# Performance work log

Hardware: AMD Instinct MI355X
Metric: run time of the kernel (lower is better)

Reference implementation:

```python
import jax, jax.numpy as jnp
import numpy as np

D_MODEL = 1024
NUM_HEADS = 16


def _linear(x, W, b):
    # torch nn.Linear: y = x @ W.T + b
    return jnp.einsum('bsd,od->bso', x, W) + b


def _split_heads(x, H):
    B, S, D = x.shape
    return x.reshape(B, S, H, D // H).transpose(0, 2, 1, 3)  # [B,H,S,dk]


def setup_inputs() -> dict:
    key0 = jax.random.key(0)
    ks = jax.random.split(key0, 11)
    B, S, D = 4, 2048, D_MODEL
    w_scale = 1.0 / np.sqrt(D)
    inp = {
        'query': jax.random.normal(ks[0], (B, S, D), jnp.float32),
        'key': jax.random.normal(ks[1], (B, S, D), jnp.float32),
        'value': jax.random.normal(ks[2], (B, S, D), jnp.float32),
        'Wq': jax.random.normal(ks[3], (D, D), jnp.float32) * w_scale,
        'bq': jax.random.normal(ks[4], (D,), jnp.float32) * 0.01,
        'Wk': jax.random.normal(ks[5], (D, D), jnp.float32) * w_scale,
        'bk': jax.random.normal(ks[6], (D,), jnp.float32) * 0.01,
        'Wv': jax.random.normal(ks[7], (D, D), jnp.float32) * w_scale,
        'bv': jax.random.normal(ks[8], (D,), jnp.float32) * 0.01,
        'Wo': jax.random.normal(ks[9], (D, D), jnp.float32) * w_scale,
        'bo': jax.random.normal(ks[10], (D,), jnp.float32) * 0.01,
        'common_prefix_len': 1792,
    }
    return inp


def reference(query, key, value, Wq, bq, Wk, bk, Wv, bv, Wo, bo, common_prefix_len):
    B, S, D = query.shape
    H = NUM_HEADS
    dk = D // H
    P = common_prefix_len
    scale = 1.0 / np.sqrt(dk)

    Q = _split_heads(_linear(query, Wq, bq), H)  # [B,H,S,dk]
    K = _split_heads(_linear(key, Wk, bk), H)
    V = _split_heads(_linear(value, Wv, bv), H)

    # --- prefix: causal self-attention over first P tokens ---
    Qp, Kp, Vp = Q[:, :, :P], K[:, :, :P], V[:, :, :P]
    sp = jnp.einsum('bhld,bhsd->bhls', Qp, Kp) * scale  # [B,H,P,P]
    causal = jnp.tril(jnp.ones((P, P), dtype=bool))
    sp = jnp.where(causal, sp, -jnp.inf)
    prefix_ctx = jnp.einsum('bhls,bhsd->bhld', jax.nn.softmax(sp, axis=-1), Vp)

    # --- candidates: attend to full prefix + own diagonal entry ---
    Qc = Q[:, :, P:]  # [B,H,N,dk]
    N = S - P
    sc = jnp.einsum('bhld,bhsd->bhls', Qc, K) * scale  # [B,H,N,S]
    mask = jnp.concatenate(
        [jnp.ones((N, P), dtype=bool), jnp.eye(N, dtype=bool)], axis=-1)  # [N,S]
    sc = jnp.where(mask, sc, -jnp.inf)
    cand_ctx = jnp.einsum('bhls,bhsd->bhld', jax.nn.softmax(sc, axis=-1), V)

    ctx = jnp.concatenate([prefix_ctx, cand_ctx], axis=2)  # [B,H,S,dk]
    ctx = ctx.transpose(0, 2, 1, 3).reshape(B, S, D)
    return _linear(ctx, Wo, bo)
```

## Files before the change

### kernel.cpp

```cpp
#include <hip/hip_runtime.h>
#include <hip/hip_bf16.h>
#include <stdint.h>
#include <stddef.h>

#define D_M   1024
#define N_H   16
#define D_K   64
#define S_LEN 2048
#define N_B   4
#define P_LEN 1792
#define M_ROWS (N_B*S_LEN)

#define QSCALE 0.1803368801111601f

typedef unsigned short u16;
typedef __bf16  bf16x8 __attribute__((ext_vector_type(8)));
typedef __bf16  bf16x4 __attribute__((ext_vector_type(4)));
typedef __bf16  bf16x2 __attribute__((ext_vector_type(2)));
typedef float   f32x4  __attribute__((ext_vector_type(4)));
typedef float   f32x16 __attribute__((ext_vector_type(16)));
typedef unsigned u32x4 __attribute__((ext_vector_type(4)));

#define MFMA32(a,b,c)   __builtin_amdgcn_mfma_f32_16x16x32_bf16((a),(b),(c),0,0,0)
#define MFMA3216(a,b,c) __builtin_amdgcn_mfma_f32_32x32x16_bf16((a),(b),(c),0,0,0)

__device__ __forceinline__ float ex2(float x){
#if defined(__HIP_DEVICE_COMPILE__) && __has_builtin(__builtin_amdgcn_exp2f)
  return __builtin_amdgcn_exp2f(x);
#else
  return exp2f(x);
#endif
}

#define GLDS16(gp, lp) __builtin_amdgcn_global_load_lds( \
    (__attribute__((address_space(1))) void*)(gp), \
    (__attribute__((address_space(3))) void*)(lp), 16, 0, 0)

__device__ __forceinline__ u16 f2bf(float f){
  unsigned u = __builtin_bit_cast(unsigned, f);
  u += 0x7FFFu + ((u>>16)&1u);
  return (u16)(u>>16);
}

__device__ __forceinline__ unsigned pkbf(float a, float b){
  bf16x2 t; t[0] = (__bf16)a; t[1] = (__bf16)b;
  return __builtin_bit_cast(unsigned, t);
}

__device__ __forceinline__ void plswap(unsigned &x, unsigned &y){
  asm("v_permlane32_swap_b32 %0, %1" : "+v"(x), "+v"(y));
}

__global__ void cvt4_bf16(const float* __restrict__ w0, const float* __restrict__ w1,
                          const float* __restrict__ w2, const float* __restrict__ w3,
                          u16* __restrict__ wqkv, u16* __restrict__ wo){
  typedef u16 u16x8 __attribute__((ext_vector_type(8)));
  const float* in = (blockIdx.y==0)? w0 : (blockIdx.y==1)? w1 : (blockIdx.y==2)? w2 : w3;
  u16* o8 = (blockIdx.y==3) ? wo : (wqkv + ((size_t)blockIdx.y << 20));
  const int i = blockIdx.x*blockDim.x + threadIdx.x;
  const float4* p = (const float4*)(in + (size_t)i*8);
  float4 a = p[0], b = p[1];
  u16x8 o;
  o[0]=f2bf(a.x); o[1]=f2bf(a.y); o[2]=f2bf(a.z); o[3]=f2bf(a.w);
  o[4]=f2bf(b.x); o[5]=f2bf(b.y); o[6]=f2bf(b.z); o[7]=f2bf(b.w);
  *(u16x8*)(o8 + (size_t)i*8) = o;
}

__global__ __launch_bounds__(256,3)
void gemm_qkv(const float* __restrict__ Aq, const float* __restrict__ Ak,
              const float* __restrict__ Av, const u16* __restrict__ W,
              const float* __restrict__ bqp, const float* __restrict__ bkp,
              const float* __restrict__ bvp,
              u16* __restrict__ Qo, u16* __restrict__ Ko, u16* __restrict__ Vo)
{
  constexpr int Kd = 1024, NT = Kd/32;
  __shared__ __align__(16) float AsF[128*32];
  __shared__ __align__(16) u16   Bs[128*32];
  const int tid  = threadIdx.x;
  const int wid  = tid >> 6, lane = tid & 63;
  const int z    = blockIdx.z;
  const int rowBase = blockIdx.x * 128, colBase = blockIdx.y * 128;

  const float* A32  = (z==0)? Aq : (z==1)? Ak : Av;
  const u16*   Bm   = W + ((size_t)z << 20);
  const float* bias = (z==0)? bqp : (z==1)? bkp : bvp;
  const float  scale = (z==0)? QSCALE : 1.0f;

  const int srow = (wid<<4) + (lane>>2);
  const int scol = (lane&3) << 3;
  const float* Asrc0 = A32 + (size_t)(rowBase + (tid>>3))*Kd
                           + (((tid&7) ^ ((tid>>3)&7)) << 2);
  const u16* Bg0 = Bm + (size_t)(colBase + srow)*Kd + scol;
  const u16* Bg1 = Bg0 + (size_t)64*Kd;
  u16* BsW0 = Bs + (wid<<9);
  u16* BsW1 = Bs + 2048 + (wid<<9);

  f32x4 acc[4][4] = {};
  const int fr = lane & 15, fk = (lane>>4) << 3;
  const int wr = (wid>>1) << 6, wc = (wid&1) << 6;

  for (int kt = 0; kt < NT; ++kt){
    const int ko = kt*32;
    __syncthreads();
#pragma unroll
    for (int g=0; g<4; ++g)
      GLDS16(Asrc0 + ko + (size_t)(32*g)*Kd, AsF + (32*g + wid*8)*32);
    GLDS16(Bg0+ko, BsW0); GLDS16(Bg1+ko, BsW1);
    __syncthreads();
    bf16x8 af[4], bf[4];
    const int hh2 = (fk>>3) << 1;
#pragma unroll
    for (int i=0;i<4;++i){
      const int rr = wr + i*16 + fr, s = rr & 7;
      const float4* rp = (const float4*)(AsF + rr*32);
      float4 lo = rp[hh2 ^ s];
      float4 hi = rp[(hh2|1) ^ s];
      af[i] = __builtin_bit_cast(bf16x8,
          (u32x4){ pkbf(lo.x,lo.y), pkbf(lo.z,lo.w),
                   pkbf(hi.x,hi.y), pkbf(hi.z,hi.w) });
    }
#pragma unroll
    for (int i=0;i<4;++i) bf[i] = *(const bf16x8*)&Bs[(wc + i*16 + fr)*32 + fk];
#pragma unroll
    for (int i=0;i<4;++i)
#pragma unroll
      for (int j=0;j<4;++j)
        acc[i][j] = MFMA32(af[i], bf[j], acc[i][j]);
  }

  const int rr0 = (lane>>4) << 2;
#pragma unroll
  for (int i=0;i<4;++i){
#pragma unroll
    for (int j=0;j<4;++j){
      const int gc = colBase + wc + j*16 + fr;
      const float bb = bias[gc];
#pragma unroll
      for (int r=0;r<4;++r){
        const int gr = rowBase + wr + i*16 + rr0 + r;
        const float v = (acc[i][j][r] + bb) * scale;
        const int b = gr >> 11, s = gr & 2047;
        const int hh = gc >> 6, k = gc & 63;
        if (z == 0){
          Qo[(((size_t)(b*N_H + hh))*S_LEN + s)*D_K + k] = f2bf(v);
        } else if (z == 1){
          const int kk = (k&7) | ((((k>>3) ^ (s&7)))<<3);
          Ko[(((size_t)(b*N_H + hh))*S_LEN + s)*D_K + kk] = f2bf(v);
        } else {
          const int ss = (s & ~63) | (s&7) | (((((s>>3)&7) ^ (k&7)))<<3);
          Vo[(((size_t)(b*N_H + hh))*D_K + k)*S_LEN + ss] = f2bf(v);
        }
      }
    }
  }
}

__global__ __launch_bounds__(256,3)
void gemm_out(const u16* __restrict__ A, const u16* __restrict__ Bm,
              const float* __restrict__ bias, float* __restrict__ Cout)
{
  constexpr int Kd = 1024, N = 1024;
  __shared__ __align__(16) u16 As[128*32];
  __shared__ __align__(16) u16 Bs[128*32];
  const int tid  = threadIdx.x;
  const int wid  = tid >> 6, lane = tid & 63;
  const int rowBase = blockIdx.x * 128, colBase = blockIdx.y * 128;

  const int srow = (wid<<4) + (lane>>2);
  const int scol = (lane&3) << 3;
  const u16* Ag0 = A  + (size_t)(rowBase + srow)*Kd + scol;
  const u16* Ag1 = Ag0 + (size_t)64*Kd;
  const u16* Bg0 = Bm + (size_t)(colBase + srow)*Kd + scol;
  const u16* Bg1 = Bg0 + (size_t)64*Kd;
  u16* AsW0 = As + (wid<<9);
  u16* AsW1 = As + 2048 + (wid<<9);
  u16* BsW0 = Bs + (wid<<9);
  u16* BsW1 = Bs + 2048 + (wid<<9);

  f32x4 acc[4][4] = {};
  const int fr = lane & 15, fk = (lane>>4) << 3;
  const int wr = (wid>>1) << 6, wc = (wid&1) << 6;

  for (int kt = 0; kt < Kd/32; ++kt){
    const int ko = kt*32;
    __syncthreads();
    GLDS16(Ag0+ko, AsW0); GLDS16(Ag1+ko, AsW1);
    GLDS16(Bg0+ko, BsW0); GLDS16(Bg1+ko, BsW1);
    __syncthreads();
    bf16x8 af[4], bf[4];
#pragma unroll
    for (int i=0;i<4;++i) af[i] = *(const bf16x8*)&As[(wr + i*16 + fr)*32 + fk];
#pragma unroll
    for (int i=0;i<4;++i) bf[i] = *(const bf16x8*)&Bs[(wc + i*16 + fr)*32 + fk];
#pragma unroll
    for (int i=0;i<4;++i)
#pragma unroll
      for (int j=0;j<4;++j)
        acc[i][j] = MFMA32(af[i], bf[j], acc[i][j]);
  }

  const int rr0 = (lane>>4) << 2;
#pragma unroll
  for (int i=0;i<4;++i){
#pragma unroll
    for (int j=0;j<4;++j){
      const int gc = colBase + wc + j*16 + fr;
      const float bb = bias[gc];
#pragma unroll
      for (int r=0;r<4;++r){
        const int gr = rowBase + wr + i*16 + rr0 + r;
        Cout[(size_t)gr*N + gc] = acc[i][j][r] + bb;
      }
    }
  }
}


__device__ __forceinline__ void attn_self(
    const u16* __restrict__ Kb, const u16* __restrict__ Vb,
    const bf16x8* qf, int ks0, int h, int q,
    float& l, f32x16& o0, f32x16& o1)
{
  bf16x8 kr[4];
  {
    const int rr = ks0 + q, sw = rr & 7;
    const u16* kp = Kb + (size_t)rr * D_K;
#pragma unroll
    for (int kb=0;kb<4;++kb)
      kr[kb] = *(const bf16x8*)(kp + (((h + 2*kb) ^ sw) << 3));
  }
  f32x16 s0 = {};
  __builtin_amdgcn_s_setprio(1);
#pragma unroll
  for (int kb=0;kb<4;++kb) s0 = MFMA3216(kr[kb], qf[kb], s0);
  __builtin_amdgcn_s_setprio(0);

  bf16x8 v0[4];
  {
    const int gb = ks0 & ~63, lc0 = (ks0 - gb) >> 3;
    const int sw = q & 7;
#pragma unroll
    for (int db=0;db<2;++db){
      const u16* vp = Vb + (size_t)(32*db + q)*S_LEN + gb;
      v0[2*db]   = *(const bf16x8*)(vp + (((lc0 + h    ) ^ sw) << 3));
      v0[2*db+1] = *(const bf16x8*)(vp + (((lc0 + h + 2) ^ sw) << 3));
    }
  }

  float a[16];
#pragma unroll
  for (int r=0;r<16;++r){
    const int krow = (r&3) + 8*(r>>2) + 4*h;
    float p0 = (krow == q) ? ex2(s0[r]) : 0.f;
    s0[r] = p0; a[r] = p0;
  }
#pragma unroll
  for (int w=8; w>=1; w>>=1)
#pragma unroll
    for (int r=0;r<w;++r) a[r] += a[r+w];
  l += a[0] + __shfl_xor(a[0], 32, 64);

  unsigned w0[8];
#pragma unroll
  for (int i=0;i<8;++i) w0[i] = pkbf(s0[2*i], s0[2*i+1]);
  plswap(w0[0],w0[2]); plswap(w0[1],w0[3]);
  plswap(w0[4],w0[6]); plswap(w0[5],w0[7]);
  bf16x8 p00 = __builtin_bit_cast(bf16x8, (u32x4){w0[0],w0[1],w0[2],w0[3]});
  bf16x8 p01 = __builtin_bit_cast(bf16x8, (u32x4){w0[4],w0[5],w0[6],w0[7]});

  __builtin_amdgcn_s_setprio(1);
  o0 = MFMA3216(v0[0], p00, o0);
  o1 = MFMA3216(v0[2], p00, o1);
  o0 = MFMA3216(v0[1], p01, o0);
  o1 = MFMA3216(v0[3], p01, o1);
  __builtin_amdgcn_s_setprio(0);
}

template<int MASKED>
__device__ __forceinline__ void steplds(
    const u16* __restrict__ Ksb, const u16* __restrict__ Vsb,
    const bf16x8* qf, bf16x8 ones, int ks, int qg, int h, int q,
    f32x16& o0, f32x16& o1, f32x16& o2)
{
  bf16x8 kr[8];
#pragma unroll
  for (int s=0;s<2;++s){
    const int rr = 32*s + q, base = rr*64, sw = rr&7;
#pragma unroll
    for (int kb=0;kb<4;++kb)
      kr[4*s+kb] = *(const bf16x8*)&Ksb[base + (((h + 2*kb)^sw)<<3)];
  }
  f32x16 s0 = {}, s1 = {};
  __builtin_amdgcn_s_setprio(1);
#pragma unroll
  for (int kb=0;kb<4;++kb){
    s0 = MFMA3216(kr[kb],   qf[kb], s0);
    s1 = MFMA3216(kr[4+kb], qf[kb], s1);
  }
  __builtin_amdgcn_s_setprio(0);

  bf16x8 v0[4], v1[4];
#pragma unroll
  for (int db=0;db<2;++db){
    const int rd = 32*db + q, base = rd*64, sw = rd&7;
    v0[2*db]   = *(const bf16x8*)&Vsb[base + (((h    )^sw)<<3)];
    v0[2*db+1] = *(const bf16x8*)&Vsb[base + (((h + 2)^sw)<<3)];
    v1[2*db]   = *(const bf16x8*)&Vsb[base + (((h + 4)^sw)<<3)];
    v1[2*db+1] = *(const bf16x8*)&Vsb[base + (((h + 6)^sw)<<3)];
  }

  if (MASKED){
#pragma unroll
    for (int r=0;r<16;++r){
      const int krow = (r&3) + 8*(r>>2) + 4*h;
      if (ks + krow      > qg) s0[r] = -1e30f;
      if (ks + 32 + krow > qg) s1[r] = -1e30f;
    }
  }

#pragma unroll
  for (int r=0;r<16;++r){ s0[r] = ex2(s0[r]); s1[r] = ex2(s1[r]); }

  unsigned w0[8];
#pragma unroll
  for (int i=0;i<8;++i) w0[i] = pkbf(s0[2*i], s0[2*i+1]);
  plswap(w0[0],w0[2]); plswap(w0[1],w0[3]);
  plswap(w0[4],w0[6]); plswap(w0[5],w0[7]);
  bf16x8 p00 = __builtin_bit_cast(bf16x8, (u32x4){w0[0],w0[1],w0[2],w0[3]});
  bf16x8 p01 = __builtin_bit_cast(bf16x8, (u32x4){w0[4],w0[5],w0[6],w0[7]});
  unsigned w1[8];
#pragma unroll
  for (int i=0;i<8;++i) w1[i] = pkbf(s1[2*i], s1[2*i+1]);
  plswap(w1[0],w1[2]); plswap(w1[1],w1[3]);
  plswap(w1[4],w1[6]); plswap(w1[5],w1[7]);
  bf16x8 p10 = __builtin_bit_cast(bf16x8, (u32x4){w1[0],w1[1],w1[2],w1[3]});
  bf16x8 p11 = __builtin_bit_cast(bf16x8, (u32x4){w1[4],w1[5],w1[6],w1[7]});

  __builtin_amdgcn_s_setprio(1);
  o0 = MFMA3216(v0[0], p00, o0);
  o1 = MFMA3216(v0[2], p00, o1);
  o2 = MFMA3216(ones,  p00, o2);
  o0 = MFMA3216(v0[1], p01, o0);
  o1 = MFMA3216(v0[3], p01, o1);
  o2 = MFMA3216(ones,  p01, o2);
  o0 = MFMA3216(v1[0], p10, o0);
  o1 = MFMA3216(v1[2], p10, o1);
  o2 = MFMA3216(ones,  p10, o2);
  o0 = MFMA3216(v1[1], p11, o0);
  o1 = MFMA3216(v1[3], p11, o1);
  o2 = MFMA3216(ones,  p11, o2);
  __builtin_amdgcn_s_setprio(0);
}

__device__ __forceinline__ void attn_write(
    u16* __restrict__ ctx, int bh, int qg, int h,
    float inv, const f32x16& o0, const f32x16& o1)
{
  const int b = bh >> 4, hd = bh & 15;
  u16* cp = ctx + ((size_t)b*S_LEN + qg)*D_M + hd*D_K;
#pragma unroll
  for (int rg=0; rg<4; ++rg){
    const int d0 = 8*rg + 4*h;
    bf16x4 oa, ob;
#pragma unroll
    for (int e=0;e<4;++e){ oa[e] = (__bf16)(o0[4*rg+e]*inv); ob[e] = (__bf16)(o1[4*rg+e]*inv); }
    *(bf16x4*)(cp + d0)      = oa;
    *(bf16x4*)(cp + 32 + d0) = ob;
  }
}

__global__ __launch_bounds__(128)
void attn_all(const u16* __restrict__ Q, const u16* __restrict__ K,
              const u16* __restrict__ Vt, u16* __restrict__ ctx)
{
  __shared__ __align__(16) u16 Ksm[2][4096];
  __shared__ __align__(16) u16 Vsm[2][4096];

  const int x = blockIdx.x;
  const int type = x >> 6, bh = x & 63;
  const int wid = threadIdx.x >> 6, lane = threadIdx.x & 63;
  const int q = lane & 31, h = lane >> 5;
  const bool iscand = (type < 4);
  const int tt = 31 - type;
  const int qb = iscand ? (P_LEN + (type<<6) + (wid<<5)) : ((tt<<6) + (wid<<5));
  const int nsteps = iscand ? (P_LEN/64) : (tt+1);
  const int qg = qb + q;

  const u16* Kb = K  + (size_t)bh * S_LEN * D_K;
  const u16* Vb = Vt + (size_t)bh * D_K * S_LEN;
  const u16* Qp = Q + ((size_t)bh * S_LEN + qg) * D_K + (h<<3);
  bf16x8 qf[4];
#pragma unroll
  for (int kb=0;kb<4;++kb) qf[kb] = *(const bf16x8*)(Qp + 16*kb);
  bf16x8 ones;
#pragma unroll
  for (int i=0;i<8;++i) ones[i] = (__bf16)1.0f;

  float lx = 0.f;
  f32x16 o0 = {}, o1 = {}, o2 = {};

  const int rl = lane >> 3, cl = (lane & 7) << 3;
  const int rb = wid << 5;

#define STAGE(T, B) do{                                                        \
    const int _ks = (T) << 6;                                                  \
    _Pragma("unroll")                                                          \
    for (int g=0; g<4; ++g){                                                   \
      const int _r = rb + (g<<3);                                              \
      GLDS16(Kb + (size_t)(_ks + _r + rl)*D_K + cl,   &Ksm[B][_r<<6]);         \
      GLDS16(Vb + (size_t)(_r + rl)*S_LEN + _ks + cl, &Vsm[B][_r<<6]);         \
    }                                                                          \
  }while(0)

  STAGE(0, 0);
  __syncthreads();

  for (int t = 0; t < nsteps; ++t){
    if (t+1 < nsteps) STAGE(t+1, (t+1)&1);
    if (!iscand && t == nsteps-1)
      steplds<1>(Ksm[t&1], Vsm[t&1], qf, ones, t<<6, qg, h, q, o0, o1, o2);
    else
      steplds<0>(Ksm[t&1], Vsm[t&1], qf, ones, t<<6, qg, h, q, o0, o1, o2);
    __syncthreads();
  }
#undef STAGE

  if (iscand)
    attn_self(Kb, Vb, qf, qb, h, q, lx, o0, o1);

  attn_write(ctx, bh, qg, h, 1.f/(o2[0] + lx), o0, o1);
}

extern "C" void kernel_launch(void* const* d_in, const int* in_sizes, int n_in,
                              void* d_out, int out_size, void* d_ws, size_t ws_size,
                              hipStream_t stream)
{
  const float* query = (const float*)d_in[0];
  const float* key   = (const float*)d_in[1];
  const float* value = (const float*)d_in[2];
  const float* Wq = (const float*)d_in[3];
  const float* bq = (const float*)d_in[4];
  const float* Wk = (const float*)d_in[5];
  const float* bk = (const float*)d_in[6];
  const float* Wv = (const float*)d_in[7];
  const float* bv = (const float*)d_in[8];
  const float* Wo = (const float*)d_in[9];
  const float* bo = (const float*)d_in[10];

  if (ws_size < (size_t)(66u<<20)) return;

  char* ws = (char*)d_ws;
  u16* Wqkv = (u16*)(ws);
  u16* ctx  = (u16*)(ws);
  u16* Wob  = (u16*)(ws + (16u<<20));
  u16* Qb   = (u16*)(ws + (18u<<20));
  u16* Kb   = (u16*)(ws + (34u<<20));
  u16* Vb   = (u16*)(ws + (50u<<20));

  dim3 gg(M_ROWS/128, D_M/128);

  cvt4_bf16<<<dim3(512,4),256,0,stream>>>(Wq, Wk, Wv, Wo, Wqkv, Wob);
  gemm_qkv<<<dim3(M_ROWS/128, D_M/128, 3),256,0,stream>>>(
      query, key, value, Wqkv, bq, bk, bv, Qb, Kb, Vb);
  attn_all<<<dim3(2048), 128, 0, stream>>>(Qb, Kb, Vb, ctx);
  gemm_out<<<gg,256,0,stream>>>(ctx, Wob, bo, (float*)d_out);
}
```

Before: 183.8 us.

## Double-buffer LDS tiles in projection GEMMs and swizzle packed QKV weights

Both the QKV projection GEMM and the output projection GEMM now keep two LDS buffers and issue the global-to-LDS loads for the next K tile before computing on the current one. This replaces the two barriers per iteration with one and is meant to hide global-load latency behind the MFMA work. Separately, the weight conversion kernel writes the QKV weights with an XOR swizzle on the 16-byte chunks, and the QKV GEMM reads B fragments with the matching swizzle to cut LDS bank conflicts. The cost is doubled LDS use per block (48KB for QKV), which may lower occupancy below the requested 3 blocks per CU.

Result: slower. 196.7 us (+7.0%).

```diff
diff --git a/kernel.cpp b/kernel.cpp
--- a/kernel.cpp
+++ b/kernel.cpp
@@ -55,15 +55,21 @@
                           const float* __restrict__ w2, const float* __restrict__ w3,
                           u16* __restrict__ wqkv, u16* __restrict__ wo){
   typedef u16 u16x8 __attribute__((ext_vector_type(8)));
-  const float* in = (blockIdx.y==0)? w0 : (blockIdx.y==1)? w1 : (blockIdx.y==2)? w2 : w3;
-  u16* o8 = (blockIdx.y==3) ? wo : (wqkv + ((size_t)blockIdx.y << 20));
+  const int y = blockIdx.y;
+  const float* in = (y==0)? w0 : (y==1)? w1 : (y==2)? w2 : w3;
   const int i = blockIdx.x*blockDim.x + threadIdx.x;
   const float4* p = (const float4*)(in + (size_t)i*8);
   float4 a = p[0], b = p[1];
   u16x8 o;
   o[0]=f2bf(a.x); o[1]=f2bf(a.y); o[2]=f2bf(a.z); o[3]=f2bf(a.w);
   o[4]=f2bf(b.x); o[5]=f2bf(b.y); o[6]=f2bf(b.z); o[7]=f2bf(b.w);
-  *(u16x8*)(o8 + (size_t)i*8) = o;
+  if (y == 3){
+    *(u16x8*)(wo + (size_t)i*8) = o;
+  } else {
+    const int n = i >> 7, c128 = i & 127;
+    const int j = (n<<7) | (c128 & ~3) | ((c128&3) ^ (n&3));
+    *(u16x8*)(wqkv + ((size_t)y<<20) + (size_t)j*8) = o;
+  }
 }
 
 __global__ __launch_bounds__(256,3)
@@ -74,8 +80,8 @@
               u16* __restrict__ Qo, u16* __restrict__ Ko, u16* __restrict__ Vo)
 {
   constexpr int Kd = 1024, NT = Kd/32;
-  __shared__ __align__(16) float AsF[128*32];
-  __shared__ __align__(16) u16   Bs[128*32];
+  __shared__ __align__(16) float AsF[2][128*32];
+  __shared__ __align__(16) u16   Bs [2][128*32];
   const int tid  = threadIdx.x;
   const int wid  = tid >> 6, lane = tid & 63;
   const int z    = blockIdx.z;
@@ -86,33 +92,37 @@
   const float* bias = (z==0)? bqp : (z==1)? bkp : bvp;
   const float  scale = (z==0)? QSCALE : 1.0f;
 
-  const int srow = (wid<<4) + (lane>>2);
-  const int scol = (lane&3) << 3;
   const float* Asrc0 = A32 + (size_t)(rowBase + (tid>>3))*Kd
                            + (((tid&7) ^ ((tid>>3)&7)) << 2);
-  const u16* Bg0 = Bm + (size_t)(colBase + srow)*Kd + scol;
-  const u16* Bg1 = Bg0 + (size_t)64*Kd;
-  u16* BsW0 = Bs + (wid<<9);
-  u16* BsW1 = Bs + 2048 + (wid<<9);
+  const int srow = (wid<<4) + (lane>>2);
+  const u16* BgBase = Bm + (size_t)(colBase + srow)*Kd + ((lane&3) << 3);
 
   f32x4 acc[4][4] = {};
   const int fr = lane & 15, fk = (lane>>4) << 3;
   const int wr = (wid>>1) << 6, wc = (wid&1) << 6;
+  const int hh2 = (lane>>4) << 1;
+
+#define STAGEG(T, B) do{                                                       \
+    const int _ko = (T)*32;                                                    \
+    _Pragma("unroll")                                                          \
+    for (int g=0; g<4; ++g)                                                    \
+      GLDS16(Asrc0 + _ko + (size_t)(32*g)*Kd, &AsF[B][(32*g + wid*8)*32]);     \
+    GLDS16(BgBase + _ko,                 &Bs[B][(wid<<9)]);                    \
+    GLDS16(BgBase + _ko + (size_t)64*Kd, &Bs[B][2048 + (wid<<9)]);             \
+  }while(0)
+
+  STAGEG(0, 0);
+  __syncthreads();
 
   for (int kt = 0; kt < NT; ++kt){
-    const int ko = kt*32;
-    __syncthreads();
-#pragma unroll
-    for (int g=0; g<4; ++g)
-      GLDS16(Asrc0 + ko + (size_t)(32*g)*Kd, AsF + (32*g + wid*8)*32);
-    GLDS16(Bg0+ko, BsW0); GLDS16(Bg1+ko, BsW1);
-    __syncthreads();
+    if (kt+1 < NT) STAGEG(kt+1, (kt+1)&1);
+    const float* Ab = AsF[kt&1];
+    const u16*   Bb = Bs [kt&1];
     bf16x8 af[4], bf[4];
-    const int hh2 = (fk>>3) << 1;
 #pragma unroll
     for (int i=0;i<4;++i){
       const int rr = wr + i*16 + fr, s = rr & 7;
-      const float4* rp = (const float4*)(AsF + rr*32);
+      const float4* rp = (const float4*)(Ab + rr*32);
       float4 lo = rp[hh2 ^ s];
       float4 hi = rp[(hh2|1) ^ s];
       af[i] = __builtin_bit_cast(bf16x8,
@@ -120,13 +130,18 @@
                    pkbf(hi.x,hi.y), pkbf(hi.z,hi.w) });
     }
 #pragma unroll
-    for (int i=0;i<4;++i) bf[i] = *(const bf16x8*)&Bs[(wc + i*16 + fr)*32 + fk];
+    for (int i=0;i<4;++i){
+      const int rr2 = wc + i*16 + fr;
+      bf[i] = *(const bf16x8*)&Bb[rr2*32 + (((fk>>3) ^ (rr2&3))<<3)];
+    }
 #pragma unroll
     for (int i=0;i<4;++i)
 #pragma unroll
       for (int j=0;j<4;++j)
         acc[i][j] = MFMA32(af[i], bf[j], acc[i][j]);
-  }
+    __syncthreads();
+  }
+#undef STAGEG
 
   const int rr0 = (lane>>4) << 2;
 #pragma unroll
@@ -159,9 +174,9 @@
 void gemm_out(const u16* __restrict__ A, const u16* __restrict__ Bm,
               const float* __restrict__ bias, float* __restrict__ Cout)
 {
-  constexpr int Kd = 1024, N = 1024;
-  __shared__ __align__(16) u16 As[128*32];
-  __shared__ __align__(16) u16 Bs[128*32];
+  constexpr int Kd = 1024, N = 1024, NT = Kd/32;
+  __shared__ __align__(16) u16 As[2][128*32];
+  __shared__ __align__(16) u16 Bs[2][128*32];
   const int tid  = threadIdx.x;
   const int wid  = tid >> 6, lane = tid & 63;
   const int rowBase = blockIdx.x * 128, colBase = blockIdx.y * 128;
@@ -172,32 +187,39 @@
   const u16* Ag1 = Ag0 + (size_t)64*Kd;
   const u16* Bg0 = Bm + (size_t)(colBase + srow)*Kd + scol;
   const u16* Bg1 = Bg0 + (size_t)64*Kd;
-  u16* AsW0 = As + (wid<<9);
-  u16* AsW1 = As + 2048 + (wid<<9);
-  u16* BsW0 = Bs + (wid<<9);
-  u16* BsW1 = Bs + 2048 + (wid<<9);
 
   f32x4 acc[4][4] = {};
   const int fr = lane & 15, fk = (lane>>4) << 3;
   const int wr = (wid>>1) << 6, wc = (wid&1) << 6;
 
-  for (int kt = 0; kt < Kd/32; ++kt){
-    const int ko = kt*32;
-    __syncthreads();
-    GLDS16(Ag0+ko, AsW0); GLDS16(Ag1+ko, AsW1);
-    GLDS16(Bg0+ko, BsW0); GLDS16(Bg1+ko, BsW1);
-    __syncthreads();
+#define STAGEO(T, B) do{                                                       \
+    const int _ko = (T)*32;                                                    \
+    GLDS16(Ag0+_ko, &As[B][(wid<<9)]);                                         \
+    GLDS16(Ag1+_ko, &As[B][2048 + (wid<<9)]);                                  \
+    GLDS16(Bg0+_ko, &Bs[B][(wid<<9)]);                                         \
+    GLDS16(Bg1+_ko, &Bs[B][2048 + (wid<<9)]);                                  \
+  }while(0)
+
+  STAGEO(0, 0);
+  __syncthreads();
+
+  for (int kt = 0; kt < NT; ++kt){
+    if (kt+1 < NT) STAGEO(kt+1, (kt+1)&1);
+    const u16* Ab = As[kt&1];
+    const u16* Bb = Bs[kt&1];
     bf16x8 af[4], bf[4];
 #pragma unroll
-    for (int i=0;i<4;++i) af[i] = *(const bf16x8*)&As[(wr + i*16 + fr)*32 + fk];
-#pragma unroll
-    for (int i=0;i<4;++i) bf[i] = *(const bf16x8*)&Bs[(wc + i*16 + fr)*32 + fk];
+    for (int i=0;i<4;++i) af[i] = *(const bf16x8*)&Ab[(wr + i*16 + fr)*32 + fk];
+#pragma unroll
+    for (int i=0;i<4;++i) bf[i] = *(const bf16x8*)&Bb[(wc + i*16 + fr)*32 + fk];
 #pragma unroll
     for (int i=0;i<4;++i)
 #pragma unroll
       for (int j=0;j<4;++j)
         acc[i][j] = MFMA32(af[i], bf[j], acc[i][j]);
-  }
+    __syncthreads();
+  }
+#undef STAGEO
 
   const int rr0 = (lane>>4) << 2;
 #pragma unroll
```
